# Kernel tuning notes

Measured on AMD Instinct MI355X. Metric: run time of the kernel, lower is better.

The kernel has to match this reference:

```python
import jax, jax.numpy as jnp
import numpy as np

B, S, D, H = 2, 2048, 1024, 16
DK = D // H


def setup_inputs() -> dict:
    key = jax.random.key(0)
    ks = jax.random.split(key, 12)
    lim = 1.0 / np.sqrt(D)
    def lin(kw, kb):
        W = jax.random.uniform(kw, (D, D), jnp.float32, -lim, lim)
        b = jax.random.uniform(kb, (D,), jnp.float32, -lim, lim)
        return W, b
    Wq, bq = lin(ks[0], ks[1])
    Wk, bk = lin(ks[2], ks[3])
    Wv, bv = lin(ks[4], ks[5])
    Wo, bo = lin(ks[6], ks[7])
    Q = jax.random.normal(ks[8], (B, S, D), jnp.float32)
    K = jax.random.normal(ks[9], (B, S, D), jnp.float32)
    V = jax.random.normal(ks[10], (B, S, D), jnp.float32)
    # causal mask, broadcastable to (B, H, S, S)
    mask = jnp.broadcast_to(jnp.tril(jnp.ones((S, S), jnp.bool_))[None, None], (B, 1, S, S))
    return {"Q": Q, "K": K, "V": V, "mask": mask,
            "Wq": Wq, "bq": bq, "Wk": Wk, "bk": bk,
            "Wv": Wv, "bv": bv, "Wo": Wo, "bo": bo}


def reference(Q, K, V, mask, Wq, bq, Wk, bk, Wv, bv, Wo, bo):
    def split(x):  # (B,S,D) -> (B,H,S,DK)
        return x.reshape(B, S, H, DK).transpose(0, 2, 1, 3)
    q = split(Q @ Wq.T + bq)
    k = split(K @ Wk.T + bk)
    v = split(V @ Wv.T + bv)
    scores = jnp.einsum('bhqd,bhkd->bhqk', q, k) / jnp.sqrt(jnp.float32(DK))
    scores = jnp.where(mask, scores, jnp.float32(-1e9))
    probs = jax.nn.softmax(scores, axis=-1)
    out = jnp.einsum('bhqk,bhkd->bhqd', probs, v)  # (B,H,S,DK)
    out = out.transpose(0, 2, 1, 3).reshape(B, S, D)
    return out @ Wo.T + bo
```

## Files before the change

### kernel.cpp

```cpp
#include <hip/hip_runtime.h>

#define S_LEN 2048
#define D_DIM 1024
#define H_NUM 16
#define DK_DIM 64
#define BATCH 2
#define M_TOT (BATCH * S_LEN)
#define XSZ 4194304
#define WSZ 1048576
#define SCALE_LOG2 0.18033688f

typedef __bf16 bf16x8 __attribute__((ext_vector_type(8)));
typedef float f32x4 __attribute__((ext_vector_type(4)));
typedef unsigned short u16;

__device__ inline u16 f2bf(float f) {
  union { float f; unsigned u; } v; v.f = f;
  unsigned u = v.u;
  return (u16)((u + 0x7FFFu + ((u >> 16) & 1u)) >> 16);
}

typedef const __attribute__((address_space(1))) unsigned int gu32;
typedef __attribute__((address_space(3))) unsigned int lu32;
__device__ inline void glds16(const u16* g, u16* l) {
  __builtin_amdgcn_global_load_lds((gu32*)g, (lu32*)l, 16, 0, 0);
}

__global__ __launch_bounds__(256)
void convert_kernel(const float* __restrict__ Q, const float* __restrict__ K,
                    const float* __restrict__ V, const float* __restrict__ Wq,
                    const float* __restrict__ Wk, const float* __restrict__ Wv,
                    const float* __restrict__ Wo, u16* __restrict__ Xb,
                    u16* __restrict__ Wb) {
  const size_t e = ((size_t)blockIdx.x * 256 + threadIdx.x) * 8;
  const float* src;
  u16* dst;
  size_t off;
  if (e < 3ull * XSZ) {
    const int a = (int)(e >> 22);
    src = (a == 0) ? Q : (a == 1) ? K : V;
    off = e - ((size_t)a << 22);
    dst = Xb + e;
  } else {
    const size_t ew = e - 3ull * XSZ;
    const int a = (int)(ew >> 20);
    src = (a == 0) ? Wq : (a == 1) ? Wk : (a == 2) ? Wv : Wo;
    off = ew - ((size_t)a << 20);
    dst = Wb + ew;
  }
  const float4 v0 = *reinterpret_cast<const float4*>(&src[off]);
  const float4 v1 = *reinterpret_cast<const float4*>(&src[off + 4]);
  ushort4 w0, w1;
  w0.x = f2bf(v0.x); w0.y = f2bf(v0.y); w0.z = f2bf(v0.z); w0.w = f2bf(v0.w);
  w1.x = f2bf(v1.x); w1.y = f2bf(v1.y); w1.z = f2bf(v1.z); w1.w = f2bf(v1.w);
  *reinterpret_cast<ushort4*>(dst) = w0;
  *reinterpret_cast<ushort4*>(dst + 4) = w1;
}

__global__ __launch_bounds__(256)
void proj_kernel(const u16* __restrict__ Qb, const u16* __restrict__ Kb,
                 const u16* __restrict__ Vb, const u16* __restrict__ Wqb,
                 const u16* __restrict__ Wkb, const u16* __restrict__ Wvb,
                 const float* __restrict__ bq, const float* __restrict__ bk,
                 const float* __restrict__ bv, u16* __restrict__ qh,
                 u16* __restrict__ kh, u16* __restrict__ vt) {
  const int z = blockIdx.z;
  const u16* A  = (z == 0) ? Qb : (z == 1) ? Kb : Vb;
  const u16* Bw = (z == 0) ? Wqb : (z == 1) ? Wkb : Wvb;
  const float* bias = (z == 0) ? bq : (z == 1) ? bk : bv;
  u16* out = (z == 0) ? qh : (z == 1) ? kh : vt;
  const float oscale = (z == 0) ? SCALE_LOG2 : 1.0f;

  __shared__ __align__(16) u16 Asm[128 * 64];
  __shared__ __align__(16) u16 Bsm[128 * 64];

  const int tid = threadIdx.x;
  const int m0 = blockIdx.x * 128, n0 = blockIdx.y * 128;
  const int wid = tid >> 6, lane = tid & 63;
  const int col = lane & 15, quad = lane >> 4;
  const int wm = (wid >> 1) * 64, wn = (wid & 1) * 64;

  const int lr = lane >> 3;
  const int lc = (lane & 7) ^ lr;
  const u16* gA = A + (size_t)(m0 + 32 * wid + lr) * D_DIM + lc * 8;
  const u16* gB = Bw + (size_t)(n0 + 32 * wid + lr) * D_DIM + lc * 8;

  f32x4 acc[4][4];
  const f32x4 zero4 = {0.f, 0.f, 0.f, 0.f};
  for (int i = 0; i < 4; i++)
    for (int j = 0; j < 4; j++) acc[i][j] = zero4;

  for (int k0 = 0; k0 < D_DIM; k0 += 64) {
    __syncthreads();
    for (int j = 0; j < 4; j++) {
      glds16(gA + (size_t)j * 8 * D_DIM + k0, &Asm[(32 * wid + 8 * j) * 64]);
      glds16(gB + (size_t)j * 8 * D_DIM + k0, &Bsm[(32 * wid + 8 * j) * 64]);
    }
    __syncthreads();

    bf16x8 af[4][2], bfm[4][2];
    for (int i = 0; i < 4; i++) {
      const int row = wm + i * 16 + col;
      const int r7 = row & 7;
      af[i][0] = *reinterpret_cast<const bf16x8*>(&Asm[row * 64 + ((quad ^ r7) * 8)]);
      af[i][1] = *reinterpret_cast<const bf16x8*>(&Asm[row * 64 + (((quad + 4) ^ r7) * 8)]);
    }
    for (int j = 0; j < 4; j++) {
      const int row = wn + j * 16 + col;
      const int r7 = row & 7;
      bfm[j][0] = *reinterpret_cast<const bf16x8*>(&Bsm[row * 64 + ((quad ^ r7) * 8)]);
      bfm[j][1] = *reinterpret_cast<const bf16x8*>(&Bsm[row * 64 + (((quad + 4) ^ r7) * 8)]);
    }
    if (z == 2) {
      for (int h = 0; h < 2; h++)
        for (int i = 0; i < 4; i++)
          for (int j = 0; j < 4; j++)
            acc[i][j] = __builtin_amdgcn_mfma_f32_16x16x32_bf16(
                af[i][h], bfm[j][h], acc[i][j], 0, 0, 0);
    } else {
      for (int h = 0; h < 2; h++)
        for (int i = 0; i < 4; i++)
          for (int j = 0; j < 4; j++)
            acc[i][j] = __builtin_amdgcn_mfma_f32_16x16x32_bf16(
                bfm[j][h], af[i][h], acc[i][j], 0, 0, 0);
    }
  }

  if (z != 2) {
    float4 b4[4];
    for (int j = 0; j < 4; j++)
      b4[j] = *reinterpret_cast<const float4*>(&bias[n0 + wn + j * 16 + quad * 4]);
    for (int i = 0; i < 4; i++) {
      const int token = m0 + wm + i * 16 + col;
      const int b = token >> 11, s = token & (S_LEN - 1);
      for (int j = 0; j < 4; j++) {
        const int gnb = n0 + wn + j * 16 + quad * 4;
        const int h = gnb >> 6, dk = gnb & 63;
        ushort4 w;
        w.x = f2bf((acc[i][j][0] + b4[j].x) * oscale);
        w.y = f2bf((acc[i][j][1] + b4[j].y) * oscale);
        w.z = f2bf((acc[i][j][2] + b4[j].z) * oscale);
        w.w = f2bf((acc[i][j][3] + b4[j].w) * oscale);
        *reinterpret_cast<ushort4*>(
            &out[((size_t)(b * H_NUM + h) * S_LEN + s) * DK_DIM + dk]) = w;
      }
    }
  } else {
    float bb[4];
    for (int j = 0; j < 4; j++) bb[j] = bias[n0 + wn + j * 16 + col];
    for (int i = 0; i < 4; i++) {
      const int token0 = m0 + wm + i * 16 + quad * 4;
      const int b = token0 >> 11, s0 = token0 & (S_LEN - 1);
      for (int j = 0; j < 4; j++) {
        const int gn = n0 + wn + j * 16 + col;
        const int h = gn >> 6, dk = gn & 63;
        ushort4 w;
        w.x = f2bf(acc[i][j][0] + bb[j]);
        w.y = f2bf(acc[i][j][1] + bb[j]);
        w.z = f2bf(acc[i][j][2] + bb[j]);
        w.w = f2bf(acc[i][j][3] + bb[j]);
        *reinterpret_cast<ushort4*>(
            &out[((size_t)(b * H_NUM + h) * DK_DIM + dk) * S_LEN + s0]) = w;
      }
    }
  }
}

__global__ __launch_bounds__(256)
void attn_kernel(const u16* __restrict__ qh, const u16* __restrict__ kh,
                 const u16* __restrict__ vt, u16* __restrict__ ctx) {
  __shared__ __align__(16) u16 Ksm[2][64 * 64];
  __shared__ __align__(16) u16 Vsm[2][64 * 64];
  __shared__ __align__(16) u16 Psm[4][16][72];

  const int tid  = threadIdx.x;
  const int flat = blockIdx.x;
  const int qb   = 31 - (flat >> 5);
  const int bh   = flat & 31;
  const int wid  = tid >> 6;
  const int lane = tid & 63;
  const int col  = lane & 15;
  const int quad = lane >> 4;
  const int r7   = col & 7;

  const int lr = lane >> 3;
  const int lc = (lane & 7) ^ lr;
  const u16* kbase = kh + ((size_t)bh * S_LEN + 16 * wid + lr) * DK_DIM + lc * 8;
  const u16* vbase = vt + ((size_t)bh * DK_DIM + 16 * wid + lr) * S_LEN + lc * 8;

  const f32x4 zero4 = {0.f, 0.f, 0.f, 0.f};
  const int b_ = bh >> 4, h_ = bh & 15;

  const int nt = qb + 1;
  const int qrow_w = qb * 64 + wid * 16;
  const int qg = qrow_w + col;

  bf16x8 qB[2];
  {
    const u16* qp = &qh[((size_t)bh * S_LEN + qg) * DK_DIM + quad * 8];
    qB[0] = *reinterpret_cast<const bf16x8*>(qp);
    qB[1] = *reinterpret_cast<const bf16x8*>(qp + 32);
  }

  glds16(kbase, &Ksm[0][(16 * wid) * 64]);
  glds16(kbase + 8 * DK_DIM, &Ksm[0][(16 * wid + 8) * 64]);
  glds16(vbase, &Vsm[0][(16 * wid) * 64]);
  glds16(vbase + (size_t)8 * S_LEN, &Vsm[0][(16 * wid + 8) * 64]);

  float l_ = 0.f;
  f32x4 o[4];
  for (int dm = 0; dm < 4; dm++) o[dm] = zero4;

  for (int tt = 0; tt < nt; tt++) {
    const int b = tt & 1;
    __syncthreads();

    if (tt + 1 < nt) {
      const int nkv = (tt + 1) * 64;
      u16* kd = &Ksm[b ^ 1][(16 * wid) * 64];
      u16* vd = &Vsm[b ^ 1][(16 * wid) * 64];
      glds16(kbase + (size_t)nkv * DK_DIM, kd);
      glds16(kbase + (size_t)(nkv + 8) * DK_DIM, kd + 8 * 64);
      glds16(vbase + nkv, vd);
      glds16(vbase + (size_t)8 * S_LEN + nkv, vd + 8 * 64);
    }

    const int kv0 = tt * 64;
    f32x4 s[4];
    __builtin_amdgcn_s_setprio(1);
    for (int nc = 0; nc < 4; nc++) {
      const int row = nc * 16 + col;
      const bf16x8 kA0 = *reinterpret_cast<const bf16x8*>(
          &Ksm[b][row * 64 + ((quad ^ r7) * 8)]);
      const bf16x8 kA1 = *reinterpret_cast<const bf16x8*>(
          &Ksm[b][row * 64 + (((quad + 4) ^ r7) * 8)]);
      f32x4 acc = zero4;
      acc = __builtin_amdgcn_mfma_f32_16x16x32_bf16(kA0, qB[0], acc, 0, 0, 0);
      acc = __builtin_amdgcn_mfma_f32_16x16x32_bf16(kA1, qB[1], acc, 0, 0, 0);
      s[nc] = acc;
    }
    __builtin_amdgcn_s_setprio(0);

    const bool domask = (kv0 + 63 > qrow_w);
    for (int nc = 0; nc < 4; nc++) {
      const int kvb = kv0 + nc * 16 + quad * 4;
      float p[4];
      for (int r = 0; r < 4; r++) {
        float e = __builtin_amdgcn_exp2f(s[nc][r]);
        if (domask && (kvb + r > qg)) e = 0.f;
        p[r] = e;
      }
      unsigned u0 = __float_as_uint(p[0]), u1 = __float_as_uint(p[1]);
      unsigned u2 = __float_as_uint(p[2]), u3 = __float_as_uint(p[3]);
      l_ += __uint_as_float(u0 & 0xffff0000u);
      l_ += __uint_as_float(u1 & 0xffff0000u);
      l_ += __uint_as_float(u2 & 0xffff0000u);
      l_ += __uint_as_float(u3 & 0xffff0000u);
      uint2 pw;
      pw.x = __builtin_amdgcn_perm(u1, u0, 0x07060302);
      pw.y = __builtin_amdgcn_perm(u3, u2, 0x07060302);
      *reinterpret_cast<uint2*>(&Psm[wid][col][nc * 16 + quad * 4]) = pw;
    }

    asm volatile("s_waitcnt lgkmcnt(0)" ::: "memory");

    bf16x8 pB[2];
    pB[0] = *reinterpret_cast<const bf16x8*>(&Psm[wid][col][quad * 8]);
    pB[1] = *reinterpret_cast<const bf16x8*>(&Psm[wid][col][32 + quad * 8]);
    __builtin_amdgcn_s_setprio(1);
    for (int dm = 0; dm < 4; dm++) {
      const int row = dm * 16 + col;
      const bf16x8 vA0 = *reinterpret_cast<const bf16x8*>(
          &Vsm[b][row * 64 + ((quad ^ r7) * 8)]);
      const bf16x8 vA1 = *reinterpret_cast<const bf16x8*>(
          &Vsm[b][row * 64 + (((quad + 4) ^ r7) * 8)]);
      o[dm] = __builtin_amdgcn_mfma_f32_16x16x32_bf16(vA0, pB[0], o[dm], 0, 0, 0);
      o[dm] = __builtin_amdgcn_mfma_f32_16x16x32_bf16(vA1, pB[1], o[dm], 0, 0, 0);
    }
    __builtin_amdgcn_s_setprio(0);
  }

  float rs = l_;
  rs += __shfl_xor(rs, 16);
  rs += __shfl_xor(rs, 32);
  const float inv = 1.0f / rs;
  for (int dm = 0; dm < 4; dm++) {
    ushort4 w;
    w.x = f2bf(o[dm][0] * inv);
    w.y = f2bf(o[dm][1] * inv);
    w.z = f2bf(o[dm][2] * inv);
    w.w = f2bf(o[dm][3] * inv);
    *reinterpret_cast<ushort4*>(
        &ctx[((size_t)b_ * S_LEN + qg) * D_DIM + h_ * DK_DIM + dm * 16 +
             quad * 4]) = w;
  }
}

__global__ __launch_bounds__(256)
void outproj_kernel(const u16* __restrict__ ctx, const u16* __restrict__ Wob,
                    const float* __restrict__ bo, float* __restrict__ out) {
  __shared__ __align__(16) u16 Asm[64 * 64];
  __shared__ __align__(16) u16 Bsm[128 * 64];

  const int tid = threadIdx.x;
  const int m0 = blockIdx.x * 64, n0 = blockIdx.y * 128;
  const int wid = tid >> 6, lane = tid & 63;
  const int col = lane & 15, quad = lane >> 4;

  const int lr = lane >> 3;
  const int lc = (lane & 7) ^ lr;
  const u16* gA = ctx + (size_t)(m0 + 16 * wid + lr) * D_DIM + lc * 8;
  const u16* gB = Wob + (size_t)(n0 + 32 * wid + lr) * D_DIM + lc * 8;

  f32x4 acc[4][2];
  const f32x4 zero4 = {0.f, 0.f, 0.f, 0.f};
  for (int i = 0; i < 4; i++)
    for (int j = 0; j < 2; j++) acc[i][j] = zero4;

  for (int k0 = 0; k0 < D_DIM; k0 += 64) {
    __syncthreads();
    for (int j = 0; j < 2; j++)
      glds16(gA + (size_t)j * 8 * D_DIM + k0, &Asm[(16 * wid + 8 * j) * 64]);
    for (int j = 0; j < 4; j++)
      glds16(gB + (size_t)j * 8 * D_DIM + k0, &Bsm[(32 * wid + 8 * j) * 64]);
    __syncthreads();

    bf16x8 af[4][2], bfm[2][2];
    for (int i = 0; i < 4; i++) {
      const int row = i * 16 + col;
      const int r7 = row & 7;
      af[i][0] = *reinterpret_cast<const bf16x8*>(&Asm[row * 64 + ((quad ^ r7) * 8)]);
      af[i][1] = *reinterpret_cast<const bf16x8*>(&Asm[row * 64 + (((quad + 4) ^ r7) * 8)]);
    }
    for (int j = 0; j < 2; j++) {
      const int row = 32 * wid + j * 16 + col;
      const int r7 = row & 7;
      bfm[j][0] = *reinterpret_cast<const bf16x8*>(&Bsm[row * 64 + ((quad ^ r7) * 8)]);
      bfm[j][1] = *reinterpret_cast<const bf16x8*>(&Bsm[row * 64 + (((quad + 4) ^ r7) * 8)]);
    }
    for (int h = 0; h < 2; h++)
      for (int i = 0; i < 4; i++)
        for (int j = 0; j < 2; j++)
          acc[i][j] = __builtin_amdgcn_mfma_f32_16x16x32_bf16(
              bfm[j][h], af[i][h], acc[i][j], 0, 0, 0);
  }

  float4 b4[2];
  for (int j = 0; j < 2; j++)
    b4[j] = *reinterpret_cast<const float4*>(
        &bo[n0 + 32 * wid + j * 16 + quad * 4]);
  for (int i = 0; i < 4; i++) {
    const int token = m0 + i * 16 + col;
    for (int j = 0; j < 2; j++) {
      const int gnb = n0 + 32 * wid + j * 16 + quad * 4;
      float4 v;
      v.x = acc[i][j][0] + b4[j].x;
      v.y = acc[i][j][1] + b4[j].y;
      v.z = acc[i][j][2] + b4[j].z;
      v.w = acc[i][j][3] + b4[j].w;
      *reinterpret_cast<float4*>(&out[(size_t)token * D_DIM + gnb]) = v;
    }
  }
}

extern "C" void kernel_launch(void* const* d_in, const int* in_sizes, int n_in,
                              void* d_out, int out_size, void* d_ws,
                              size_t ws_size, hipStream_t stream) {
  const float* Q  = (const float*)d_in[0];
  const float* K  = (const float*)d_in[1];
  const float* V  = (const float*)d_in[2];
  const float* Wq = (const float*)d_in[4];
  const float* bq = (const float*)d_in[5];
  const float* Wk = (const float*)d_in[6];
  const float* bk = (const float*)d_in[7];
  const float* Wv = (const float*)d_in[8];
  const float* bv = (const float*)d_in[9];
  const float* Wo = (const float*)d_in[10];
  const float* bo = (const float*)d_in[11];
  float* out = (float*)d_out;

  u16* qh  = (u16*)d_ws;
  u16* kh  = qh + XSZ;
  u16* vt  = kh + XSZ;
  u16* Qb  = vt + XSZ;
  u16* ctx = Qb;
  u16* Kb  = Qb + XSZ;
  u16* Vb  = Kb + XSZ;
  u16* Wqb = Vb + XSZ;
  u16* Wkb = Wqb + WSZ;
  u16* Wvb = Wkb + WSZ;
  u16* Wob = Wvb + WSZ;

  convert_kernel<<<(3 * XSZ + 4 * WSZ) / (256 * 8), 256, 0, stream>>>(
      Q, K, V, Wq, Wk, Wv, Wo, Qb, Wqb);

  proj_kernel<<<dim3(M_TOT / 128, D_DIM / 128, 3), 256, 0, stream>>>(
      Qb, Kb, Vb, Wqb, Wkb, Wvb, bq, bk, bv, qh, kh, vt);

  attn_kernel<<<dim3(1024), 256, 0, stream>>>(qh, kh, vt, ctx);

  outproj_kernel<<<dim3(M_TOT / 64, D_DIM / 128), 256, 0, stream>>>(ctx, Wob,
                                                                    bo, out);
}
```

Baseline: 240.3 us.

## Double-buffer LDS tiles in the projection GEMM kernels to prefetch the next K-slice

Both the QKV projection and output projection kernels now keep two LDS buffers for the A and B tiles. Before the loop they load the first K-slice. Each iteration then issues the direct global-to-LDS load for the next slice before reading the current one, so one barrier per step replaces two. The goal is to hide global load latency behind the MFMA work. In exchange, LDS use per block doubles, which may lower occupancy. If the compiler inserts a full vmcnt wait before the LDS reads, the overlap could also be lost.

Result: no change. 238.6 us (-0.7%).

```diff
diff --git a/kernel.cpp b/kernel.cpp
--- a/kernel.cpp
+++ b/kernel.cpp
@@ -71,8 +71,8 @@
   u16* out = (z == 0) ? qh : (z == 1) ? kh : vt;
   const float oscale = (z == 0) ? SCALE_LOG2 : 1.0f;
 
-  __shared__ __align__(16) u16 Asm[128 * 64];
-  __shared__ __align__(16) u16 Bsm[128 * 64];
+  __shared__ __align__(16) u16 Asm[2][128 * 64];
+  __shared__ __align__(16) u16 Bsm[2][128 * 64];
 
   const int tid = threadIdx.x;
   const int m0 = blockIdx.x * 128, n0 = blockIdx.y * 128;
@@ -90,26 +90,37 @@
   for (int i = 0; i < 4; i++)
     for (int j = 0; j < 4; j++) acc[i][j] = zero4;
 
-  for (int k0 = 0; k0 < D_DIM; k0 += 64) {
+  for (int j = 0; j < 4; j++) {
+    glds16(gA + (size_t)j * 8 * D_DIM, &Asm[0][(32 * wid + 8 * j) * 64]);
+    glds16(gB + (size_t)j * 8 * D_DIM, &Bsm[0][(32 * wid + 8 * j) * 64]);
+  }
+
+  for (int ks = 0; ks < 16; ks++) {
+    const int b = ks & 1;
     __syncthreads();
-    for (int j = 0; j < 4; j++) {
-      glds16(gA + (size_t)j * 8 * D_DIM + k0, &Asm[(32 * wid + 8 * j) * 64]);
-      glds16(gB + (size_t)j * 8 * D_DIM + k0, &Bsm[(32 * wid + 8 * j) * 64]);
-    }
-    __syncthreads();
+
+    if (ks + 1 < 16) {
+      const int k1 = (ks + 1) * 64;
+      for (int j = 0; j < 4; j++) {
+        glds16(gA + (size_t)j * 8 * D_DIM + k1,
+               &Asm[b ^ 1][(32 * wid + 8 * j) * 64]);
+        glds16(gB + (size_t)j * 8 * D_DIM + k1,
+               &Bsm[b ^ 1][(32 * wid + 8 * j) * 64]);
+      }
+    }
 
     bf16x8 af[4][2], bfm[4][2];
     for (int i = 0; i < 4; i++) {
       const int row = wm + i * 16 + col;
       const int r7 = row & 7;
-      af[i][0] = *reinterpret_cast<const bf16x8*>(&Asm[row * 64 + ((quad ^ r7) * 8)]);
-      af[i][1] = *reinterpret_cast<const bf16x8*>(&Asm[row * 64 + (((quad + 4) ^ r7) * 8)]);
+      af[i][0] = *reinterpret_cast<const bf16x8*>(&Asm[b][row * 64 + ((quad ^ r7) * 8)]);
+      af[i][1] = *reinterpret_cast<const bf16x8*>(&Asm[b][row * 64 + (((quad + 4) ^ r7) * 8)]);
     }
     for (int j = 0; j < 4; j++) {
       const int row = wn + j * 16 + col;
       const int r7 = row & 7;
-      bfm[j][0] = *reinterpret_cast<const bf16x8*>(&Bsm[row * 64 + ((quad ^ r7) * 8)]);
-      bfm[j][1] = *reinterpret_cast<const bf16x8*>(&Bsm[row * 64 + (((quad + 4) ^ r7) * 8)]);
+      bfm[j][0] = *reinterpret_cast<const bf16x8*>(&Bsm[b][row * 64 + ((quad ^ r7) * 8)]);
+      bfm[j][1] = *reinterpret_cast<const bf16x8*>(&Bsm[b][row * 64 + (((quad + 4) ^ r7) * 8)]);
     }
     if (z == 2) {
       for (int h = 0; h < 2; h++)
@@ -299,8 +310,8 @@
 __global__ __launch_bounds__(256)
 void outproj_kernel(const u16* __restrict__ ctx, const u16* __restrict__ Wob,
                     const float* __restrict__ bo, float* __restrict__ out) {
-  __shared__ __align__(16) u16 Asm[64 * 64];
-  __shared__ __align__(16) u16 Bsm[128 * 64];
+  __shared__ __align__(16) u16 Asm[2][64 * 64];
+  __shared__ __align__(16) u16 Bsm[2][128 * 64];
 
   const int tid = threadIdx.x;
   const int m0 = blockIdx.x * 64, n0 = blockIdx.y * 128;
@@ -317,26 +328,37 @@
   for (int i = 0; i < 4; i++)
     for (int j = 0; j < 2; j++) acc[i][j] = zero4;
 
-  for (int k0 = 0; k0 < D_DIM; k0 += 64) {
+  for (int j = 0; j < 2; j++)
+    glds16(gA + (size_t)j * 8 * D_DIM, &Asm[0][(16 * wid + 8 * j) * 64]);
+  for (int j = 0; j < 4; j++)
+    glds16(gB + (size_t)j * 8 * D_DIM, &Bsm[0][(32 * wid + 8 * j) * 64]);
+
+  for (int ks = 0; ks < 16; ks++) {
+    const int b = ks & 1;
     __syncthreads();
-    for (int j = 0; j < 2; j++)
-      glds16(gA + (size_t)j * 8 * D_DIM + k0, &Asm[(16 * wid + 8 * j) * 64]);
-    for (int j = 0; j < 4; j++)
-      glds16(gB + (size_t)j * 8 * D_DIM + k0, &Bsm[(32 * wid + 8 * j) * 64]);
-    __syncthreads();
+
+    if (ks + 1 < 16) {
+      const int k1 = (ks + 1) * 64;
+      for (int j = 0; j < 2; j++)
+        glds16(gA + (size_t)j * 8 * D_DIM + k1,
+               &Asm[b ^ 1][(16 * wid + 8 * j) * 64]);
+      for (int j = 0; j < 4; j++)
+        glds16(gB + (size_t)j * 8 * D_DIM + k1,
+               &Bsm[b ^ 1][(32 * wid + 8 * j) * 64]);
+    }
 
     bf16x8 af[4][2], bfm[2][2];
     for (int i = 0; i < 4; i++) {
       const int row = i * 16 + col;
       const int r7 = row & 7;
-      af[i][0] = *reinterpret_cast<const bf16x8*>(&Asm[row * 64 + ((quad ^ r7) * 8)]);
-      af[i][1] = *reinterpret_cast<const bf16x8*>(&Asm[row * 64 + (((quad + 4) ^ r7) * 8)]);
+      af[i][0] = *reinterpret_cast<const bf16x8*>(&Asm[b][row * 64 + ((quad ^ r7) * 8)]);
+      af[i][1] = *reinterpret_cast<const bf16x8*>(&Asm[b][row * 64 + (((quad + 4) ^ r7) * 8)]);
     }
     for (int j = 0; j < 2; j++) {
       const int row = 32 * wid + j * 16 + col;
       const int r7 = row & 7;
-      bfm[j][0] = *reinterpret_cast<const bf16x8*>(&Bsm[row * 64 + ((quad ^ r7) * 8)]);
-      bfm[j][1] = *reinterpret_cast<const bf16x8*>(&Bsm[row * 64 + (((quad + 4) ^ r7) * 8)]);
+      bfm[j][0] = *reinterpret_cast<const bf16x8*>(&Bsm[b][row * 64 + ((quad ^ r7) * 8)]);
+      bfm[j][1] = *reinterpret_cast<const bf16x8*>(&Bsm[b][row * 64 + (((quad + 4) ^ r7) * 8)]);
     }
     for (int h = 0; h < 2; h++)
       for (int i = 0; i < 4; i++)
```

## Fuse fp32-to-bf16 conversion into projection GEMM loads and swizzle P buffer

Applied to the files above, without the earlier changes.

Removes the separate conversion kernel. The projection and output-projection GEMMs now load fp32 inputs and weights directly, convert them to bf16 in registers and store into swizzled LDS, replacing the async global-to-LDS copies. This drops a full read/write pass over the activations and weights plus one launch. In exchange each GEMM reads twice as many bytes per tile and loses the async LDS loads. Separately, the attention P buffer drops its padding in favour of an XOR swizzle, and the causal query-block order is changed to interleave heavy and light blocks.

Result: slower. 419.5 us (+74.6%).

```diff
diff --git a/kernel.cpp b/kernel.cpp
--- a/kernel.cpp
+++ b/kernel.cpp
@@ -7,7 +7,6 @@
 #define BATCH 2
 #define M_TOT (BATCH * S_LEN)
 #define XSZ 4194304
-#define WSZ 1048576
 #define SCALE_LOG2 0.18033688f
 
 typedef __bf16 bf16x8 __attribute__((ext_vector_type(8)));
@@ -26,47 +25,23 @@
   __builtin_amdgcn_global_load_lds((gu32*)g, (lu32*)l, 16, 0, 0);
 }
 
-__global__ __launch_bounds__(256)
-void convert_kernel(const float* __restrict__ Q, const float* __restrict__ K,
-                    const float* __restrict__ V, const float* __restrict__ Wq,
-                    const float* __restrict__ Wk, const float* __restrict__ Wv,
-                    const float* __restrict__ Wo, u16* __restrict__ Xb,
-                    u16* __restrict__ Wb) {
-  const size_t e = ((size_t)blockIdx.x * 256 + threadIdx.x) * 8;
-  const float* src;
-  u16* dst;
-  size_t off;
-  if (e < 3ull * XSZ) {
-    const int a = (int)(e >> 22);
-    src = (a == 0) ? Q : (a == 1) ? K : V;
-    off = e - ((size_t)a << 22);
-    dst = Xb + e;
-  } else {
-    const size_t ew = e - 3ull * XSZ;
-    const int a = (int)(ew >> 20);
-    src = (a == 0) ? Wq : (a == 1) ? Wk : (a == 2) ? Wv : Wo;
-    off = ew - ((size_t)a << 20);
-    dst = Wb + ew;
-  }
-  const float4 v0 = *reinterpret_cast<const float4*>(&src[off]);
-  const float4 v1 = *reinterpret_cast<const float4*>(&src[off + 4]);
-  ushort4 w0, w1;
-  w0.x = f2bf(v0.x); w0.y = f2bf(v0.y); w0.z = f2bf(v0.z); w0.w = f2bf(v0.w);
-  w1.x = f2bf(v1.x); w1.y = f2bf(v1.y); w1.z = f2bf(v1.z); w1.w = f2bf(v1.w);
-  *reinterpret_cast<ushort4*>(dst) = w0;
-  *reinterpret_cast<ushort4*>(dst + 4) = w1;
-}
-
-__global__ __launch_bounds__(256)
-void proj_kernel(const u16* __restrict__ Qb, const u16* __restrict__ Kb,
-                 const u16* __restrict__ Vb, const u16* __restrict__ Wqb,
-                 const u16* __restrict__ Wkb, const u16* __restrict__ Wvb,
+__device__ inline bf16x8 cvt8(const float4& a, const float4& b) {
+  bf16x8 w;
+  w[0] = (__bf16)a.x; w[1] = (__bf16)a.y; w[2] = (__bf16)a.z; w[3] = (__bf16)a.w;
+  w[4] = (__bf16)b.x; w[5] = (__bf16)b.y; w[6] = (__bf16)b.z; w[7] = (__bf16)b.w;
+  return w;
+}
+
+__global__ __launch_bounds__(256, 3)
+void proj_kernel(const float* __restrict__ Qf, const float* __restrict__ Kf,
+                 const float* __restrict__ Vf, const float* __restrict__ Wqf,
+                 const float* __restrict__ Wkf, const float* __restrict__ Wvf,
                  const float* __restrict__ bq, const float* __restrict__ bk,
                  const float* __restrict__ bv, u16* __restrict__ qh,
                  u16* __restrict__ kh, u16* __restrict__ vt) {
   const int z = blockIdx.z;
-  const u16* A  = (z == 0) ? Qb : (z == 1) ? Kb : Vb;
-  const u16* Bw = (z == 0) ? Wqb : (z == 1) ? Wkb : Wvb;
+  const float* A  = (z == 0) ? Qf : (z == 1) ? Kf : Vf;
+  const float* Bw = (z == 0) ? Wqf : (z == 1) ? Wkf : Wvf;
   const float* bias = (z == 0) ? bq : (z == 1) ? bk : bv;
   u16* out = (z == 0) ? qh : (z == 1) ? kh : vt;
   const float oscale = (z == 0) ? SCALE_LOG2 : 1.0f;
@@ -81,9 +56,10 @@
   const int wm = (wid >> 1) * 64, wn = (wid & 1) * 64;
 
   const int lr = lane >> 3;
-  const int lc = (lane & 7) ^ lr;
-  const u16* gA = A + (size_t)(m0 + 32 * wid + lr) * D_DIM + lc * 8;
-  const u16* gB = Bw + (size_t)(n0 + 32 * wid + lr) * D_DIM + lc * 8;
+  const int lq = lane & 7;
+  const int lc = lq ^ lr;
+  const float* gA = A + (size_t)(m0 + 32 * wid + lr) * D_DIM + lc * 8;
+  const float* gB = Bw + (size_t)(n0 + 32 * wid + lr) * D_DIM + lc * 8;
 
   f32x4 acc[4][4];
   const f32x4 zero4 = {0.f, 0.f, 0.f, 0.f};
@@ -93,8 +69,18 @@
   for (int k0 = 0; k0 < D_DIM; k0 += 64) {
     __syncthreads();
     for (int j = 0; j < 4; j++) {
-      glds16(gA + (size_t)j * 8 * D_DIM + k0, &Asm[(32 * wid + 8 * j) * 64]);
-      glds16(gB + (size_t)j * 8 * D_DIM + k0, &Bsm[(32 * wid + 8 * j) * 64]);
+      const float4 a0 = *reinterpret_cast<const float4*>(
+          &gA[(size_t)j * 8 * D_DIM + k0]);
+      const float4 a1 = *reinterpret_cast<const float4*>(
+          &gA[(size_t)j * 8 * D_DIM + k0 + 4]);
+      const float4 b0 = *reinterpret_cast<const float4*>(
+          &gB[(size_t)j * 8 * D_DIM + k0]);
+      const float4 b1 = *reinterpret_cast<const float4*>(
+          &gB[(size_t)j * 8 * D_DIM + k0 + 4]);
+      *reinterpret_cast<bf16x8*>(
+          &Asm[(32 * wid + 8 * j + lr) * 64 + lq * 8]) = cvt8(a0, a1);
+      *reinterpret_cast<bf16x8*>(
+          &Bsm[(32 * wid + 8 * j + lr) * 64 + lq * 8]) = cvt8(b0, b1);
     }
     __syncthreads();
 
@@ -171,17 +157,19 @@
                  const u16* __restrict__ vt, u16* __restrict__ ctx) {
   __shared__ __align__(16) u16 Ksm[2][64 * 64];
   __shared__ __align__(16) u16 Vsm[2][64 * 64];
-  __shared__ __align__(16) u16 Psm[4][16][72];
+  __shared__ __align__(16) u16 Psm[4][16][64];
 
   const int tid  = threadIdx.x;
   const int flat = blockIdx.x;
-  const int qb   = 31 - (flat >> 5);
+  const int g    = flat >> 5;
+  const int qb   = (g < 16) ? (31 - g) : (g - 16);
   const int bh   = flat & 31;
   const int wid  = tid >> 6;
   const int lane = tid & 63;
   const int col  = lane & 15;
   const int quad = lane >> 4;
   const int r7   = col & 7;
+  const int psw  = (col & 3) << 4;
 
   const int lr = lane >> 3;
   const int lc = (lane & 7) ^ lr;
@@ -259,14 +247,16 @@
       uint2 pw;
       pw.x = __builtin_amdgcn_perm(u1, u0, 0x07060302);
       pw.y = __builtin_amdgcn_perm(u3, u2, 0x07060302);
-      *reinterpret_cast<uint2*>(&Psm[wid][col][nc * 16 + quad * 4]) = pw;
+      *reinterpret_cast<uint2*>(
+          &Psm[wid][col][(nc * 16 + quad * 4) ^ psw]) = pw;
     }
 
     asm volatile("s_waitcnt lgkmcnt(0)" ::: "memory");
 
     bf16x8 pB[2];
-    pB[0] = *reinterpret_cast<const bf16x8*>(&Psm[wid][col][quad * 8]);
-    pB[1] = *reinterpret_cast<const bf16x8*>(&Psm[wid][col][32 + quad * 8]);
+    pB[0] = *reinterpret_cast<const bf16x8*>(&Psm[wid][col][(quad * 8) ^ psw]);
+    pB[1] = *reinterpret_cast<const bf16x8*>(
+        &Psm[wid][col][(32 + quad * 8) ^ psw]);
     __builtin_amdgcn_s_setprio(1);
     for (int dm = 0; dm < 4; dm++) {
       const int row = dm * 16 + col;
@@ -297,7 +287,7 @@
 }
 
 __global__ __launch_bounds__(256)
-void outproj_kernel(const u16* __restrict__ ctx, const u16* __restrict__ Wob,
+void outproj_kernel(const u16* __restrict__ ctx, const float* __restrict__ Wof,
                     const float* __restrict__ bo, float* __restrict__ out) {
   __shared__ __align__(16) u16 Asm[64 * 64];
   __shared__ __align__(16) u16 Bsm[128 * 64];
@@ -308,9 +298,10 @@
   const int col = lane & 15, quad = lane >> 4;
 
   const int lr = lane >> 3;
-  const int lc = (lane & 7) ^ lr;
+  const int lq = lane & 7;
+  const int lc = lq ^ lr;
   const u16* gA = ctx + (size_t)(m0 + 16 * wid + lr) * D_DIM + lc * 8;
-  const u16* gB = Wob + (size_t)(n0 + 32 * wid + lr) * D_DIM + lc * 8;
+  const float* gB = Wof + (size_t)(n0 + 32 * wid + lr) * D_DIM + lc * 8;
 
   f32x4 acc[4][2];
   const f32x4 zero4 = {0.f, 0.f, 0.f, 0.f};
@@ -321,8 +312,14 @@
     __syncthreads();
     for (int j = 0; j < 2; j++)
       glds16(gA + (size_t)j * 8 * D_DIM + k0, &Asm[(16 * wid + 8 * j) * 64]);
-    for (int j = 0; j < 4; j++)
-      glds16(gB + (size_t)j * 8 * D_DIM + k0, &Bsm[(32 * wid + 8 * j) * 64]);
+    for (int j = 0; j < 4; j++) {
+      const float4 b0 = *reinterpret_cast<const float4*>(
+          &gB[(size_t)j * 8 * D_DIM + k0]);
+      const float4 b1 = *reinterpret_cast<const float4*>(
+          &gB[(size_t)j * 8 * D_DIM + k0 + 4]);
+      *reinterpret_cast<bf16x8*>(
+          &Bsm[(32 * wid + 8 * j + lr) * 64 + lq * 8]) = cvt8(b0, b1);
+    }
     __syncthreads();
 
     bf16x8 af[4][2], bfm[2][2];
@@ -382,23 +379,13 @@
   u16* qh  = (u16*)d_ws;
   u16* kh  = qh + XSZ;
   u16* vt  = kh + XSZ;
-  u16* Qb  = vt + XSZ;
-  u16* ctx = Qb;
-  u16* Kb  = Qb + XSZ;
-  u16* Vb  = Kb + XSZ;
-  u16* Wqb = Vb + XSZ;
-  u16* Wkb = Wqb + WSZ;
-  u16* Wvb = Wkb + WSZ;
-  u16* Wob = Wvb + WSZ;
-
-  convert_kernel<<<(3 * XSZ + 4 * WSZ) / (256 * 8), 256, 0, stream>>>(
-      Q, K, V, Wq, Wk, Wv, Wo, Qb, Wqb);
+  u16* ctx = vt + XSZ;
 
   proj_kernel<<<dim3(M_TOT / 128, D_DIM / 128, 3), 256, 0, stream>>>(
-      Qb, Kb, Vb, Wqb, Wkb, Wvb, bq, bk, bv, qh, kh, vt);
+      Q, K, V, Wq, Wk, Wv, bq, bk, bv, qh, kh, vt);
 
   attn_kernel<<<dim3(1024), 256, 0, stream>>>(qh, kh, vt, ctx);
 
-  outproj_kernel<<<dim3(M_TOT / 64, D_DIM / 128), 256, 0, stream>>>(ctx, Wob,
+  outproj_kernel<<<dim3(M_TOT / 64, D_DIM / 128), 256, 0, stream>>>(ctx, Wo,
                                                                     bo, out);
 }
```
